# Performance work log

Hardware: AMD Instinct MI355X
Metric: run time of the kernel (lower is better)

## Reference

```python
import jax, jax.numpy as jnp
import numpy as np

N = 100_000      # atom_count
E = 6_400_000    # number of (directed) edges, avg degree 64
BOX = 100.0      # simulation box edge length


def setup_inputs() -> dict:
    key = jax.random.key(0)
    k1, k2, k3 = jax.random.split(key, 3)
    pos = jax.random.uniform(k1, (N, 3), dtype=jnp.float32) * BOX
    src = jax.random.randint(k2, (E,), 0, N, dtype=jnp.int32)
    # offset in [1, N) guarantees dst != src (no zero-distance self edges)
    off = jax.random.randint(k3, (E,), 1, N, dtype=jnp.int32)
    dst = ((src + off) % N).astype(jnp.int32)
    edge_index = jnp.stack([src, dst], axis=0)  # [2, E]
    sigma = jnp.asarray(0.3, dtype=jnp.float32)
    epsilon = jnp.asarray(1.0, dtype=jnp.float32)
    return {"pos": pos, "sigma": sigma, "epsilon": epsilon, "edge_index": edge_index}


def _total_energy(pos, sigma, epsilon, src, dst):
    # r = edge_attr: per-edge distance, differentiable w.r.t. pos
    d = pos[src] - pos[dst]                      # [E, 3] gather + subtract
    r = jnp.sqrt(jnp.sum(d * d, axis=-1))        # [E]
    sr6 = (sigma / r) ** 6
    # potential_formula: 4*epsilon*((sigma/r)**12 - (sigma/r)**6)
    v_r = 4.0 * epsilon * (sr6 * sr6 - sr6)      # [E]
    return v_r.sum()


def reference(pos, sigma, epsilon, edge_index):
    src, dst = edge_index[0], edge_index[1]
    energy = _total_energy(pos, sigma, epsilon, src, dst)
    # afc: autograd force — grad of summed pair potential w.r.t. positions
    # (per-edge force scattered onto atoms by edge_index; grad does the
    #  gather-compute-scatter in one pass)
    pair_force = jax.grad(_total_energy, argnums=0)(pos, sigma, epsilon, src, dst)
    atom_force = -pair_force / 2.0               # /2: each pair counted twice
    return energy, atom_force
```

## Files before the change

kernel.cpp:

```cpp
#include <hip/hip_runtime.h>


#define BIN_SHIFT 11
#define BIN_ATOMS 2048
#define FNBINS    49
#define SLABF     (BIN_ATOMS * 3)
#define NBLKA     500
#define EPB       12800
#define RBLOCK    512
#define CAPR      1024
#define NCHUNK    10
#define BPC       (NBLKA / NCHUNK)
#define NACC      (FNBINS * NCHUNK)

__global__ __launch_bounds__(256) void pf_pad(
    const float* __restrict__ pos, float4* __restrict__ pos4, int N)
{
    const int i = blockIdx.x * 256 + threadIdx.x;
    if (i < N)
        pos4[i] = make_float4(pos[3 * i + 0], pos[3 * i + 1], pos[3 * i + 2], 0.f);
}

__global__ __launch_bounds__(RBLOCK) void pf_route(
    const int* __restrict__ src, const int* __restrict__ dst,
    unsigned* __restrict__ gbuf,
    int* __restrict__ gcnt)
{
    __shared__ int cur[FNBINS];
    const int t   = threadIdx.x;
    const int blk = blockIdx.x;
    if (t < FNBINS) cur[t] = 0;
    __syncthreads();

    const int base = blk * EPB;
    const int4* s4p = (const int4*)(src + base);
    const int4* d4p = (const int4*)(dst + base);

    for (int q = t; q < EPB / 4; q += RBLOCK) {
        const int4 s4 = s4p[q];
        const int4 d4 = d4p[q];
        #pragma unroll
        for (int k = 0; k < 4; ++k) {
            const int s = (k == 0) ? s4.x : (k == 1) ? s4.y : (k == 2) ? s4.z : s4.w;
            const int d = (k == 0) ? d4.x : (k == 1) ? d4.y : (k == 2) ? d4.z : d4.w;
            const int b0 = s >> BIN_SHIFT;
            const unsigned r0 = ((unsigned)(s & (BIN_ATOMS - 1)) << 17) | (unsigned)d;
            const int p0 = atomicAdd(&cur[b0], 1);
            if (p0 < CAPR)
                gbuf[((size_t)b0 * NBLKA + blk) * CAPR + p0] = r0;
            const int b1 = d >> BIN_SHIFT;
            const unsigned r1 = ((unsigned)(d & (BIN_ATOMS - 1)) << 17) | (unsigned)s;
            const int p1 = atomicAdd(&cur[b1], 1);
            if (p1 < CAPR)
                gbuf[((size_t)b1 * NBLKA + blk) * CAPR + p1] = r1;
        }
    }
    __syncthreads();
    if (t < FNBINS) gcnt[t * NBLKA + blk] = min(cur[t], CAPR);
}

__global__ __launch_bounds__(1024) void pf_accum(
    const float*  __restrict__ pos,
    const float4* __restrict__ pos4,
    const float*  __restrict__ sigma_p, const float* __restrict__ eps_p,
    const unsigned* __restrict__ gbuf,
    const int* __restrict__ gcnt,
    float* __restrict__ srow,
    float* __restrict__ erep,
    int N)
{
    extern __shared__ float sh[];
    const int t = threadIdx.x;
    const int b = blockIdx.x / NCHUNK;
    const int c = blockIdx.x % NCHUNK;

    for (int j = t; j < SLABF / 4; j += 1024)
        ((float4*)sh)[j] = make_float4(0.f, 0.f, 0.f, 0.f);
    const int binStart = b << BIN_SHIFT;
    const int nb = min(BIN_ATOMS, N - binStart);
    for (int j = t; j < nb * 3; j += 1024)
        sh[SLABF + j] = pos[binStart * 3 + j];
    if (t < 16) sh[2 * SLABF + t] = 0.f;
    __syncthreads();

    const float sigma = sigma_p[0];
    const float eps   = eps_p[0];
    const float sig2  = sigma * sigma;

    const int w    = t >> 6;
    const int lane = t & 63;

    float ev = 0.f;
    for (int sbi = w; sbi < BPC; sbi += 16) {
        const int bucket = b * NBLKA + c * BPC + sbi;
        const int n = gcnt[bucket];
        const unsigned* buf = gbuf + (size_t)bucket * CAPR;
        for (int j = lane; j < n; j += 64) {
            const unsigned r = buf[j];
            const int la    = (int)(r >> 17);
            const int other = (int)(r & 0x1ffffu);

            const float4 op = pos4[other];
            const float dx = sh[SLABF + 3 * la + 0] - op.x;
            const float dy = sh[SLABF + 3 * la + 1] - op.y;
            const float dz = sh[SLABF + 3 * la + 2] - op.z;

            const float r2     = dx * dx + dy * dy + dz * dz;
            const float inv_r2 = 1.0f / r2;
            const float s2     = sig2 * inv_r2;
            const float sr6    = s2 * s2 * s2;
            const float sr12   = sr6 * sr6;

            ev += 4.0f * eps * (sr12 - sr6);
            const float fs = 12.0f * eps * (2.0f * sr12 - sr6) * inv_r2;

            atomicAdd(&sh[3 * la + 0], fs * dx);
            atomicAdd(&sh[3 * la + 1], fs * dy);
            atomicAdd(&sh[3 * la + 2], fs * dz);
        }
    }

    #pragma unroll
    for (int off = 32; off > 0; off >>= 1)
        ev += __shfl_down(ev, off, 64);
    if (lane == 0) sh[2 * SLABF + w] = ev;
    __syncthreads();

    float4* row = (float4*)(srow + (size_t)blockIdx.x * SLABF);
    for (int j = t; j < SLABF / 4; j += 1024)
        row[j] = ((float4*)sh)[j];

    if (t == 0) {
        float e = 0.f;
        #pragma unroll
        for (int q = 0; q < 16; ++q) e += sh[2 * SLABF + q];
        erep[blockIdx.x] = e;
    }
}

__global__ __launch_bounds__(256) void pf_reduce(
    const float* __restrict__ srow, const float* __restrict__ erep,
    float* __restrict__ out, int n3)
{
    const int g = blockIdx.x * 256 + threadIdx.x;
    if (g < n3) {
        const int a    = g / 3;
        const int comp = g - 3 * a;
        const int b    = a >> BIN_SHIFT;
        const int la   = a & (BIN_ATOMS - 1);
        float acc = 0.f;
        #pragma unroll 5
        for (int c = 0; c < NCHUNK; ++c)
            acc += srow[(size_t)(b * NCHUNK + c) * SLABF + 3 * la + comp];
        out[1 + g] = acc;
    }
    if (blockIdx.x == 0) {
        float e = 0.f;
        for (int j = threadIdx.x; j < NACC; j += 256) e += erep[j];
        #pragma unroll
        for (int off = 32; off > 0; off >>= 1) e += __shfl_down(e, off, 64);
        __shared__ float ep[4];
        if ((threadIdx.x & 63) == 0) ep[threadIdx.x >> 6] = e;
        __syncthreads();
        if (threadIdx.x == 0)
            out[0] = 0.5f * (ep[0] + ep[1] + ep[2] + ep[3]);
    }
}

#define NBINS8     8
#define BINA8      12800
#define BINF8      (BINA8 * 3)
#define ROWF8      (NBINS8 * BINF8)
#define BLOCK8     1024
#define MAXCHUNKS8 32

__global__ __launch_bounds__(BLOCK8, 1) void pairforce_binned(
    const float* __restrict__ pos,
    const float* __restrict__ sigma_p,
    const float* __restrict__ eps_p,
    const int*   __restrict__ src,
    const int*   __restrict__ dst,
    float* __restrict__ frep, float* __restrict__ erep,
    int nEdges, int chunkEdges)
{
    extern __shared__ float sh[];
    const int t = threadIdx.x;
    const int b = blockIdx.x % NBINS8;
    const int c = blockIdx.x / NBINS8;

    for (int j = t; j < (BINF8 + 16) / 4; j += BLOCK8)
        ((float4*)sh)[j] = make_float4(0.f, 0.f, 0.f, 0.f);
    __syncthreads();

    const float sigma = sigma_p[0];
    const float eps   = eps_p[0];
    const float sig2  = sigma * sigma;
    const int binStart = b * BINA8;

    const int start = c * chunkEdges;
    const int end   = min(start + chunkEdges, nEdges);

    const int4* src4 = (const int4*)src;
    const int4* dst4 = (const int4*)dst;

    float ev = 0.0f;
    for (int i4 = (start >> 2) + t; i4 < (end >> 2); i4 += BLOCK8) {
        const int4 s4 = src4[i4];
        const int4 d4 = dst4[i4];
        #pragma unroll
        for (int k = 0; k < 4; ++k) {
            const int s = (k == 0) ? s4.x : (k == 1) ? s4.y : (k == 2) ? s4.z : s4.w;
            const int d = (k == 0) ? d4.x : (k == 1) ? d4.y : (k == 2) ? d4.z : d4.w;
            const unsigned ls = (unsigned)(s - binStart);
            const unsigned ld = (unsigned)(d - binStart);
            const bool hs = ls < BINA8;
            const bool hd = ld < BINA8;
            if (hs | hd) {
                const float dx = pos[3 * s + 0] - pos[3 * d + 0];
                const float dy = pos[3 * s + 1] - pos[3 * d + 1];
                const float dz = pos[3 * s + 2] - pos[3 * d + 2];
                const float r2     = dx * dx + dy * dy + dz * dz;
                const float inv_r2 = 1.0f / r2;
                const float s2v    = sig2 * inv_r2;
                const float sr6    = s2v * s2v * s2v;
                const float sr12   = sr6 * sr6;
                const float fsc = 12.0f * eps * (2.0f * sr12 - sr6) * inv_r2;
                const float fx = fsc * dx, fy = fsc * dy, fz = fsc * dz;
                if (hs) {
                    atomicAdd(&sh[3 * ls + 0],  fx);
                    atomicAdd(&sh[3 * ls + 1],  fy);
                    atomicAdd(&sh[3 * ls + 2],  fz);
                    ev += 4.0f * eps * (sr12 - sr6);
                }
                if (hd) {
                    atomicAdd(&sh[3 * ld + 0], -fx);
                    atomicAdd(&sh[3 * ld + 1], -fy);
                    atomicAdd(&sh[3 * ld + 2], -fz);
                }
            }
        }
    }

    #pragma unroll
    for (int off = 32; off > 0; off >>= 1)
        ev += __shfl_down(ev, off, 64);
    if ((t & 63) == 0) sh[BINF8 + (t >> 6)] = ev;
    __syncthreads();

    float4* outSeg = (float4*)(frep + (size_t)c * ROWF8 + (size_t)b * BINF8);
    for (int j = t; j < BINF8 / 4; j += BLOCK8)
        outSeg[j] = ((float4*)sh)[j];

    if (t == 0) {
        float e = 0.f;
        #pragma unroll
        for (int q = 0; q < 16; ++q) e += sh[BINF8 + q];
        erep[blockIdx.x] = e;
    }
}

__global__ __launch_bounds__(256) void pairforce_reduce8(
    const float* __restrict__ frep, const float* __restrict__ erep,
    float* __restrict__ out, int n3, int nChunks, int nPart)
{
    const int i = blockIdx.x * 256 + threadIdx.x;
    if (i < n3) {
        float acc = 0.f;
        for (int c = 0; c < nChunks; ++c)
            acc += frep[(size_t)c * ROWF8 + i];
        out[1 + i] = acc;
    }
    if (blockIdx.x == gridDim.x - 1) {
        float e = 0.f;
        for (int j = threadIdx.x; j < nPart; j += 256) e += erep[j];
        #pragma unroll
        for (int off = 32; off > 0; off >>= 1) e += __shfl_down(e, off, 64);
        __shared__ float ep[4];
        if ((threadIdx.x & 63) == 0) ep[threadIdx.x >> 6] = e;
        __syncthreads();
        if (threadIdx.x == 0) out[0] = ep[0] + ep[1] + ep[2] + ep[3];
    }
}

extern "C" void kernel_launch(void* const* d_in, const int* in_sizes, int n_in,
                              void* d_out, int out_size, void* d_ws, size_t ws_size,
                              hipStream_t stream)
{
    const float* pos     = (const float*)d_in[0];
    const float* sigma_p = (const float*)d_in[1];
    const float* eps_p   = (const float*)d_in[2];
    const int*   edge    = (const int*)d_in[3];

    const int nEdges = in_sizes[3] / 2;
    const int* src = edge;
    const int* dst = edge + nEdges;

    const int n3 = out_size - 1;
    const int N  = n3 / 3;

    const size_t gbufBytes = (size_t)FNBINS * NBLKA * CAPR * sizeof(unsigned);
    const size_t pos4Bytes = (size_t)100000 * sizeof(float4);
    const size_t srowBytes = (size_t)NACC * SLABF * sizeof(float);
    const size_t gcntBytes = (size_t)FNBINS * NBLKA * sizeof(int);
    const size_t erepBytes = (size_t)NACC * sizeof(float);
    const size_t needFast  = gbufBytes + pos4Bytes + srowBytes + gcntBytes +
                             erepBytes + 256;
    const bool fastOK = (N == 100000) && (nEdges == NBLKA * EPB) &&
                        (ws_size >= needFast);

    if (fastOK) {
        char* p = (char*)d_ws;
        unsigned* gbuf = (unsigned*)p;           p += gbufBytes;
        float4*   pos4 = (float4*)p;             p += pos4Bytes;
        float*    srow = (float*)p;              p += srowBytes;
        int*      gcnt = (int*)p;                p += gcntBytes;
        float*    erep = (float*)p;

        pf_pad<<<(N + 255) / 256, 256, 0, stream>>>(pos, pos4, N);

        pf_route<<<NBLKA, RBLOCK, 0, stream>>>(src, dst, gbuf, gcnt);

        const size_t shB = (2 * SLABF + 16) * sizeof(float);
        pf_accum<<<NACC, 1024, shB, stream>>>(pos, pos4, sigma_p, eps_p,
                                              gbuf, gcnt, srow, erep, N);

        pf_reduce<<<(n3 + 255) / 256, 256, 0, stream>>>(srow, erep,
                                                        (float*)d_out, n3);
        return;
    }

    const size_t rowBytes = (size_t)ROWF8 * sizeof(float);
    int nChunks = (int)((ws_size - 4096) / rowBytes);
    if (nChunks > MAXCHUNKS8) nChunks = MAXCHUNKS8;
    if (nChunks < 1) nChunks = 1;
    const int chunkEdges = (((nEdges + nChunks - 1) / nChunks) + 3) & ~3;

    float* frep = (float*)d_ws;
    float* erep = frep + (size_t)nChunks * ROWF8;

    const size_t shbytes = (size_t)(BINF8 + 16) * sizeof(float);
    pairforce_binned<<<nChunks * NBINS8, BLOCK8, shbytes, stream>>>(
        pos, sigma_p, eps_p, src, dst, frep, erep, nEdges, chunkEdges);

    pairforce_reduce8<<<(n3 + 255) / 256, 256, 0, stream>>>(
        frep, erep, (float*)d_out, n3, nChunks, nChunks * NBINS8);
}
```

Baseline: 359.3 us.

## Vectorize bucket reads with sentinel padding and retune routing/chunk partitioning

Each route bucket is padded to a multiple of four with a sentinel index that points at far-away padded positions, so the accumulate kernel can read four packed edge records with one uint4 load and issue four independent position gathers before the math. The local bin positions are now kept in shared memory as float4 copied from the padded pos4 array. The block and chunk counts are also retuned (512 route blocks of 1024 threads, 16 chunks per bin), and the sub-bucket loop is unrolled. Sentinel edges add a little wasted math, and the extra chunks raise the size of the partial-sum array and the reduce traffic.

```diff
diff --git a/kernel.cpp b/kernel.cpp
--- a/kernel.cpp
+++ b/kernel.cpp
@@ -5,13 +5,15 @@
 #define BIN_ATOMS 2048
 #define FNBINS    49
 #define SLABF     (BIN_ATOMS * 3)
-#define NBLKA     500
-#define EPB       12800
-#define RBLOCK    512
+#define NBLKA     512
+#define EPB       12500
+#define RBLOCK    1024
 #define CAPR      1024
-#define NCHUNK    10
+#define NCHUNK    16
 #define BPC       (NBLKA / NCHUNK)
 #define NACC      (FNBINS * NCHUNK)
+#define NPAD      102400
+#define SENT      100000u
 
 __global__ __launch_bounds__(256) void pf_pad(
     const float* __restrict__ pos, float4* __restrict__ pos4, int N)
@@ -19,6 +21,8 @@
     const int i = blockIdx.x * 256 + threadIdx.x;
     if (i < N)
         pos4[i] = make_float4(pos[3 * i + 0], pos[3 * i + 1], pos[3 * i + 2], 0.f);
+    else if (i < NPAD)
+        pos4[i] = make_float4(1e18f, 1e18f, 1e18f, 0.f);
 }
 
 __global__ __launch_bounds__(RBLOCK) void pf_route(
@@ -56,11 +60,36 @@
         }
     }
     __syncthreads();
-    if (t < FNBINS) gcnt[t * NBLKA + blk] = min(cur[t], CAPR);
+    if (t < FNBINS) {
+        int n = min(cur[t], CAPR);
+        unsigned* buf = gbuf + ((size_t)t * NBLKA + blk) * CAPR;
+        while ((n & 3) && n < CAPR) { buf[n] = SENT; ++n; }
+        gcnt[t * NBLKA + blk] = n;
+    }
+}
+
+__device__ __forceinline__ void lj_body(
+    unsigned r, const float4* __restrict__ shp4, float* __restrict__ slab,
+    const float4 P, float sig2, float eps, float& ev)
+{
+    const int la = (int)(r >> 17);
+    const float4 Q = shp4[la];
+    const float dx = Q.x - P.x;
+    const float dy = Q.y - P.y;
+    const float dz = Q.z - P.z;
+    const float r2     = dx * dx + dy * dy + dz * dz;
+    const float inv_r2 = 1.0f / r2;
+    const float s2     = sig2 * inv_r2;
+    const float sr6    = s2 * s2 * s2;
+    const float sr12   = sr6 * sr6;
+    ev += 4.0f * eps * (sr12 - sr6);
+    const float fs = 12.0f * eps * (2.0f * sr12 - sr6) * inv_r2;
+    atomicAdd(&slab[3 * la + 0], fs * dx);
+    atomicAdd(&slab[3 * la + 1], fs * dy);
+    atomicAdd(&slab[3 * la + 2], fs * dz);
 }
 
 __global__ __launch_bounds__(1024) void pf_accum(
-    const float*  __restrict__ pos,
     const float4* __restrict__ pos4,
     const float*  __restrict__ sigma_p, const float* __restrict__ eps_p,
     const unsigned* __restrict__ gbuf,
@@ -70,6 +99,9 @@
     int N)
 {
     extern __shared__ float sh[];
+    float4* shp4  = (float4*)(sh + SLABF);
+    float*  epart = sh + SLABF + 4 * BIN_ATOMS;
+
     const int t = threadIdx.x;
     const int b = blockIdx.x / NCHUNK;
     const int c = blockIdx.x % NCHUNK;
@@ -78,9 +110,9 @@
         ((float4*)sh)[j] = make_float4(0.f, 0.f, 0.f, 0.f);
     const int binStart = b << BIN_SHIFT;
     const int nb = min(BIN_ATOMS, N - binStart);
-    for (int j = t; j < nb * 3; j += 1024)
-        sh[SLABF + j] = pos[binStart * 3 + j];
-    if (t < 16) sh[2 * SLABF + t] = 0.f;
+    for (int j = t; j < nb; j += 1024)
+        shp4[j] = pos4[binStart + j];
+    if (t < 16) epart[t] = 0.f;
     __syncthreads();
 
     const float sigma = sigma_p[0];
@@ -91,39 +123,29 @@
     const int lane = t & 63;
 
     float ev = 0.f;
-    for (int sbi = w; sbi < BPC; sbi += 16) {
-        const int bucket = b * NBLKA + c * BPC + sbi;
+    #pragma unroll
+    for (int sbi = 0; sbi < BPC / 16; ++sbi) {
+        const int sb     = c * BPC + sbi * 16 + w;
+        const int bucket = b * NBLKA + sb;
         const int n = gcnt[bucket];
         const unsigned* buf = gbuf + (size_t)bucket * CAPR;
-        for (int j = lane; j < n; j += 64) {
-            const unsigned r = buf[j];
-            const int la    = (int)(r >> 17);
-            const int other = (int)(r & 0x1ffffu);
-
-            const float4 op = pos4[other];
-            const float dx = sh[SLABF + 3 * la + 0] - op.x;
-            const float dy = sh[SLABF + 3 * la + 1] - op.y;
-            const float dz = sh[SLABF + 3 * la + 2] - op.z;
-
-            const float r2     = dx * dx + dy * dy + dz * dz;
-            const float inv_r2 = 1.0f / r2;
-            const float s2     = sig2 * inv_r2;
-            const float sr6    = s2 * s2 * s2;
-            const float sr12   = sr6 * sr6;
-
-            ev += 4.0f * eps * (sr12 - sr6);
-            const float fs = 12.0f * eps * (2.0f * sr12 - sr6) * inv_r2;
-
-            atomicAdd(&sh[3 * la + 0], fs * dx);
-            atomicAdd(&sh[3 * la + 1], fs * dy);
-            atomicAdd(&sh[3 * la + 2], fs * dz);
+        for (int j = lane * 4; j < n; j += 256) {
+            const uint4 r4 = *(const uint4*)(buf + j);
+            const float4 P0 = pos4[r4.x & 0x1ffffu];
+            const float4 P1 = pos4[r4.y & 0x1ffffu];
+            const float4 P2 = pos4[r4.z & 0x1ffffu];
+            const float4 P3 = pos4[r4.w & 0x1ffffu];
+            lj_body(r4.x, shp4, sh, P0, sig2, eps, ev);
+            lj_body(r4.y, shp4, sh, P1, sig2, eps, ev);
+            lj_body(r4.z, shp4, sh, P2, sig2, eps, ev);
+            lj_body(r4.w, shp4, sh, P3, sig2, eps, ev);
         }
     }
 
     #pragma unroll
     for (int off = 32; off > 0; off >>= 1)
         ev += __shfl_down(ev, off, 64);
-    if (lane == 0) sh[2 * SLABF + w] = ev;
+    if (lane == 0) epart[w] = ev;
     __syncthreads();
 
     float4* row = (float4*)(srow + (size_t)blockIdx.x * SLABF);
@@ -133,7 +155,7 @@
     if (t == 0) {
         float e = 0.f;
         #pragma unroll
-        for (int q = 0; q < 16; ++q) e += sh[2 * SLABF + q];
+        for (int q = 0; q < 16; ++q) e += epart[q];
         erep[blockIdx.x] = e;
     }
 }
@@ -149,7 +171,7 @@
         const int b    = a >> BIN_SHIFT;
         const int la   = a & (BIN_ATOMS - 1);
         float acc = 0.f;
-        #pragma unroll 5
+        #pragma unroll 4
         for (int c = 0; c < NCHUNK; ++c)
             acc += srow[(size_t)(b * NCHUNK + c) * SLABF + 3 * la + comp];
         out[1 + g] = acc;
@@ -299,7 +321,7 @@
     const int N  = n3 / 3;
 
     const size_t gbufBytes = (size_t)FNBINS * NBLKA * CAPR * sizeof(unsigned);
-    const size_t pos4Bytes = (size_t)100000 * sizeof(float4);
+    const size_t pos4Bytes = (size_t)NPAD * sizeof(float4);
     const size_t srowBytes = (size_t)NACC * SLABF * sizeof(float);
     const size_t gcntBytes = (size_t)FNBINS * NBLKA * sizeof(int);
     const size_t erepBytes = (size_t)NACC * sizeof(float);
@@ -316,12 +338,12 @@
         int*      gcnt = (int*)p;                p += gcntBytes;
         float*    erep = (float*)p;
 
-        pf_pad<<<(N + 255) / 256, 256, 0, stream>>>(pos, pos4, N);
+        pf_pad<<<(NPAD + 255) / 256, 256, 0, stream>>>(pos, pos4, N);
 
         pf_route<<<NBLKA, RBLOCK, 0, stream>>>(src, dst, gbuf, gcnt);
 
-        const size_t shB = (2 * SLABF + 16) * sizeof(float);
-        pf_accum<<<NACC, 1024, shB, stream>>>(pos, pos4, sigma_p, eps_p,
+        const size_t shB = (SLABF + 4 * BIN_ATOMS + 16) * sizeof(float);
+        pf_accum<<<NACC, 1024, shB, stream>>>(pos4, sigma_p, eps_p,
                                               gbuf, gcnt, srow, erep, N);
 
         pf_reduce<<<(n3 + 255) / 256, 256, 0, stream>>>(srow, erep,
```

Result: slower. 416.8 us (+16.0%).
